# Kernel optimization log

Measured on AMD Instinct MI355X. Metric: run time of the kernel, lower is better.

## Reference

```python
import jax, jax.numpy as jnp
import numpy as np

N = 40000      # nodes
E = 640000     # edges (avg degree 16)
F = 128        # in_feats
OUT = 128      # out_feats


def setup_inputs() -> dict:
    key = jax.random.key(0)
    ks = jax.random.split(key, 8)
    feat = jax.random.normal(ks[0], (N, F), dtype=jnp.float32)
    src = jax.random.randint(ks[1], (E,), 0, N, dtype=jnp.int32)
    dst = jnp.sort(jax.random.randint(ks[2], (E,), 0, N, dtype=jnp.int32))
    # AttentionAGG: fc1 (2F -> F), fc2 (F -> 1); fc_layer (2F -> OUT)
    s1 = 1.0 / np.sqrt(2 * F)
    s2 = 1.0 / np.sqrt(F)
    w1 = jax.random.normal(ks[3], (2 * F, F), dtype=jnp.float32) * s1
    b1 = jnp.zeros((F,), dtype=jnp.float32)
    w2 = jax.random.normal(ks[4], (F, 1), dtype=jnp.float32) * s2
    b2 = jnp.zeros((1,), dtype=jnp.float32)
    wf = jax.random.normal(ks[5], (2 * F, OUT), dtype=jnp.float32) * s1
    bf = jnp.zeros((OUT,), dtype=jnp.float32)
    return {"feat": feat, "src": src, "dst": dst,
            "w1": w1, "b1": b1, "w2": w2, "b2": b2, "wf": wf, "bf": bf}


def reference(feat, src, dst, w1, b1, w2, b2, wf, bf):
    f = feat.shape[1]
    n = feat.shape[0]
    # fc1(concat(h_dst, m_src)) == h_dst @ w1[:F] + h_src @ w1[F:]  (edge_weight is None)
    proj_dst = feat @ w1[:f]          # [N, F]
    proj_src = feat @ w1[f:]          # [N, F]
    pre = jnp.tanh(proj_dst[dst] + proj_src[src] + b1)   # [E, F]
    scores = (pre @ w2)[:, 0] + b2[0]                    # [E]
    # softmax over the ragged incoming-edge set of each dst node
    smax = jax.ops.segment_max(scores, dst, num_segments=n, indices_are_sorted=True)
    ex = jnp.exp(scores - jax.lax.stop_gradient(smax)[dst])
    den = jax.ops.segment_sum(ex, dst, num_segments=n, indices_are_sorted=True)
    att = ex / den[dst]                                  # [E]
    # weighted segment-sum of messages (m_e = feat[src]); zero-degree nodes get 0
    neigh = jax.ops.segment_sum(att[:, None] * feat[src], dst,
                                num_segments=n, indices_are_sorted=True)  # [N, F]
    # fc_layer(concat(h_self, neigh))
    rst = feat @ wf[:f] + neigh @ wf[f:] + bf            # [N, OUT]
    return rst
```

## Files before the change

### kernel.cpp

```cpp
#include <hip/hip_runtime.h>
#include <math.h>

#define F 128
#define OUT 128

typedef unsigned short ushort_t;
typedef __attribute__((ext_vector_type(8))) short bfrag;
typedef __attribute__((ext_vector_type(4))) float ffrag;

__device__ __forceinline__ float bf_lo(unsigned int u) {
    return __uint_as_float(u << 16);
}
__device__ __forceinline__ float bf_hi(unsigned int u) {
    return __uint_as_float(u & 0xffff0000u);
}
__device__ __forceinline__ ushort_t f2bf(float f) {
    unsigned int x = __float_as_uint(f);
    unsigned int r = x + 0x7fffu + ((x >> 16) & 1u);
    return (ushort_t)(r >> 16);
}
__device__ __forceinline__ unsigned pk2(float lo, float hi) {
    return (unsigned)f2bf(lo) | ((unsigned)f2bf(hi) << 16);
}

#define DPP_ADD(x, ctrl) \
    ((x) + __int_as_float(__builtin_amdgcn_update_dpp( \
        0, __float_as_int(x), (ctrl), 0xf, 0xf, true)))

__global__ __launch_bounds__(256) void prep_kernel(
    const float* __restrict__ feat, const float* __restrict__ w1,
    const float* __restrict__ wf, const int* __restrict__ dst,
    ushort_t* __restrict__ abig, ushort_t* __restrict__ srcpack,
    ushort_t* __restrict__ btp, ushort_t* __restrict__ btf,
    int* __restrict__ row_ptr, int n, int e, int nb0, int nb1, int nb2)
{
    const int b = blockIdx.x, t = threadIdx.x;
    if (b < nb0) {
        int i = b * 256 + t;
        if (i >= n * 16) return;
        int row = i >> 4, c = (i & 15) * 8;
        float4 a = *(const float4*)(feat + (size_t)row * F + c);
        float4 bb = *(const float4*)(feat + (size_t)row * F + c + 4);
        unsigned p0 = pk2(a.x, a.y), p1 = pk2(a.z, a.w);
        unsigned p2 = pk2(bb.x, bb.y), p3 = pk2(bb.z, bb.w);
        *(uint4*)(abig + (size_t)row * 256 + c) = make_uint4(p0, p1, p2, p3);
        *(uint2*)(srcpack + (size_t)row * 256 + c * 2 + 4) = make_uint2(p0, p1);
        *(uint2*)(srcpack + (size_t)row * 256 + c * 2 + 12) = make_uint2(p2, p3);
    } else if (b < nb0 + nb1) {
        int idx = (b - nb0) * 256 + t;
        int j = idx >> 7, k = idx & 127;
        float v = (j < F) ? w1[(size_t)k * F + j]
                          : w1[(size_t)(F + k) * F + (j - F)];
        btp[idx] = f2bf(v);
    } else if (b < nb0 + nb1 + nb2) {
        int idx = (b - nb0 - nb1) * 256 + t;
        int j = idx >> 8, k = idx & 255;
        btf[idx] = f2bf(wf[(size_t)k * F + j]);
    } else {
        int i = (b - nb0 - nb1 - nb2) * 256 + t;
        if (i >= e) return;
        int d = dst[i];
        int prev = (i == 0) ? -1 : dst[i - 1];
        for (int v = prev + 1; v <= d; ++v) row_ptr[v] = i;
        if (i == e - 1) {
            for (int v = d + 1; v <= n; ++v) row_ptr[v] = e;
        }
    }
}

#define PST 136
__global__ __launch_bounds__(256) void proj_gemm_kernel(
    const ushort_t* __restrict__ abig, const ushort_t* __restrict__ btp,
    const float* __restrict__ b1, ushort_t* __restrict__ e_dst,
    ushort_t* __restrict__ srcpack, int n)
{
    __shared__ ushort_t As[64 * PST];
    __shared__ ushort_t Ep[4][16 * 80];
    const int t = threadIdx.x;
    const int wv = t >> 6, lane = t & 63;
    const int lm = lane & 15, quad = lane >> 4;
    const int row0 = blockIdx.x * 64, col0 = wv * 64;

#pragma unroll
    for (int k = 0; k < 4; ++k) {
        int l = k * 256 + t;
        int r = l >> 4, ch = l & 15;
        uint4 d = make_uint4(0, 0, 0, 0);
        if (row0 + r < n) d = *(const uint4*)(abig + (size_t)(row0 + r) * 256 + ch * 8);
        *(uint4*)(As + r * PST + ch * 8) = d;
    }
    __syncthreads();

    bfrag bfr[4][4];
#pragma unroll
    for (int ks = 0; ks < 4; ++ks)
#pragma unroll
        for (int ni = 0; ni < 4; ++ni)
            bfr[ks][ni] = *(const bfrag*)(btp + (size_t)(col0 + ni * 16 + lm) * 128
                                          + ks * 32 + quad * 8);

    ffrag acc[4][4];
#pragma unroll
    for (int mi = 0; mi < 4; ++mi)
#pragma unroll
        for (int ni = 0; ni < 4; ++ni) acc[mi][ni] = (ffrag){0.f, 0.f, 0.f, 0.f};

#pragma unroll
    for (int ks = 0; ks < 4; ++ks)
#pragma unroll
        for (int mi = 0; mi < 4; ++mi) {
            bfrag af = *(const bfrag*)(As + (mi * 16 + lm) * PST + ks * 32 + quad * 8);
#pragma unroll
            for (int ni = 0; ni < 4; ++ni)
                acc[mi][ni] = __builtin_amdgcn_mfma_f32_16x16x32_bf16(
                    af, bfr[ks][ni], acc[mi][ni], 0, 0, 0);
        }

    float bias[4];
#pragma unroll
    for (int ni = 0; ni < 4; ++ni)
        bias[ni] = (col0 < F) ? b1[col0 + ni * 16 + lm] : 0.f;

#pragma unroll
    for (int mi = 0; mi < 4; ++mi) {
#pragma unroll
        for (int ni = 0; ni < 4; ++ni)
#pragma unroll
            for (int r = 0; r < 4; ++r)
                Ep[wv][(quad * 4 + r) * 80 + ni * 16 + lm] =
                    f2bf(__expf(2.f * (acc[mi][ni][r] + bias[ni])));
#pragma unroll
        for (int ps = 0; ps < 2; ++ps) {
            int rl = ps * 8 + (lane >> 3), co = (lane & 7) * 8;
            uint4 vv = *(const uint4*)(&Ep[wv][rl * 80 + co]);
            int grow = row0 + mi * 16 + rl;
            if (grow < n) {
                if (col0 < F) {
                    *(uint4*)(e_dst + (size_t)grow * F + col0 + co) = vv;
                } else {
                    int f0 = col0 - F + co;
                    *(uint2*)(srcpack + (size_t)grow * 256 + f0 * 2) =
                        make_uint2(vv.x, vv.y);
                    *(uint2*)(srcpack + (size_t)grow * 256 + f0 * 2 + 8) =
                        make_uint2(vv.z, vv.w);
                }
            }
        }
    }
}

__global__ __launch_bounds__(256) void fused_kernel(
    const ushort_t* __restrict__ e_dst, const ushort_t* __restrict__ srcpack,
    const int* __restrict__ src, const int* __restrict__ row_ptr,
    const float* __restrict__ w2, ushort_t* __restrict__ abig, int n)
{
    const int v = (int)((blockIdx.x * 256u + threadIdx.x) >> 5);
    const int fl = threadIdx.x & 31;
    const int sbase = threadIdx.x & 32;

    const float4 wv4 = ((const float4*)w2)[fl];
    const float w0 = wv4.x, w1_ = wv4.y, w2_ = wv4.z, w3_ = wv4.w;
    float sw = w0 + w1_ + w2_ + w3_;
    float aw = fabsf(w0) + fabsf(w1_) + fabsf(w2_) + fabsf(w3_);
#pragma unroll
    for (int off = 16; off; off >>= 1) {
        sw += __shfl_xor(sw, off, 64);
        aw += __shfl_xor(aw, off, 64);
    }
    const float K = sw - aw;
    const float L2E = 1.4426950408889634f;
    const float K2 = K * L2E;

    if (v >= n) return;
    const int begin = row_ptr[v], end = row_ptr[v + 1];

    const uint2 ud = *(const uint2*)(e_dst + (size_t)v * F + fl * 4);
    const float ea0 = bf_lo(ud.x), ea1 = bf_hi(ud.x);
    const float ea2 = bf_lo(ud.y), ea3 = bf_hi(ud.y);

    const uint4* __restrict__ sp = (const uint4*)srcpack + fl;

    float s = 0.f, a0 = 0.f, a1 = 0.f, a2 = 0.f, a3 = 0.f;

    for (int cb = begin; cb < end; cb += 32) {
        const int clen = min(32, end - cb);
        const int sv = (fl < clen) ? src[cb + fl] : 0;
        int jj = 0;
        uint4 u[4];
        if (jj + 4 <= clen) {
#pragma unroll
            for (int q = 0; q < 4; ++q) {
                const int sq = __shfl(sv, sbase + q, 64);
                u[q] = sp[(size_t)sq * 32];
            }
        }
        while (jj + 4 <= clen) {
            const int jn = jj + 4;
            uint4 un[4];
            if (jn + 4 <= clen) {
#pragma unroll
                for (int q = 0; q < 4; ++q) {
                    const int sq = __shfl(sv, sbase + jn + q, 64);
                    un[q] = sp[(size_t)sq * 32];
                }
            }
            float p[4];
#pragma unroll
            for (int q = 0; q < 4; ++q) {
                float r;
                r = __builtin_amdgcn_rcpf(fmaf(ea0, bf_lo(u[q].x), 1.f)); p[q] = w0 * r;
                r = __builtin_amdgcn_rcpf(fmaf(ea1, bf_hi(u[q].x), 1.f)); p[q] = fmaf(w1_, r, p[q]);
                r = __builtin_amdgcn_rcpf(fmaf(ea2, bf_lo(u[q].y), 1.f)); p[q] = fmaf(w2_, r, p[q]);
                r = __builtin_amdgcn_rcpf(fmaf(ea3, bf_hi(u[q].y), 1.f)); p[q] = fmaf(w3_, r, p[q]);
            }
#pragma unroll
            for (int q = 0; q < 4; ++q) {
                p[q] = DPP_ADD(p[q], 0x121);
                p[q] = DPP_ADD(p[q], 0x122);
                p[q] = DPP_ADD(p[q], 0x124);
                p[q] = DPP_ADD(p[q], 0x128);
                p[q] += __shfl_xor(p[q], 16, 64);
            }
            float g[4];
#pragma unroll
            for (int q = 0; q < 4; ++q)
                g[q] = exp2f(fmaf(-2.f * L2E, p[q], K2));
            s += (g[0] + g[1]) + (g[2] + g[3]);
#pragma unroll
            for (int q = 0; q < 4; ++q) {
                a0 = fmaf(g[q], bf_lo(u[q].z), a0);
                a1 = fmaf(g[q], bf_hi(u[q].z), a1);
                a2 = fmaf(g[q], bf_lo(u[q].w), a2);
                a3 = fmaf(g[q], bf_hi(u[q].w), a3);
            }
            jj = jn;
            if (jj + 4 <= clen) {
#pragma unroll
                for (int q = 0; q < 4; ++q) u[q] = un[q];
            }
        }
        for (; jj < clen; ++jj) {
            const int s0 = __shfl(sv, sbase + jj, 64);
            const uint4 u0 = sp[(size_t)s0 * 32];
            float r, p0;
            r = __builtin_amdgcn_rcpf(fmaf(ea0, bf_lo(u0.x), 1.f)); p0 = w0 * r;
            r = __builtin_amdgcn_rcpf(fmaf(ea1, bf_hi(u0.x), 1.f)); p0 = fmaf(w1_, r, p0);
            r = __builtin_amdgcn_rcpf(fmaf(ea2, bf_lo(u0.y), 1.f)); p0 = fmaf(w2_, r, p0);
            r = __builtin_amdgcn_rcpf(fmaf(ea3, bf_hi(u0.y), 1.f)); p0 = fmaf(w3_, r, p0);
            p0 = DPP_ADD(p0, 0x121);
            p0 = DPP_ADD(p0, 0x122);
            p0 = DPP_ADD(p0, 0x124);
            p0 = DPP_ADD(p0, 0x128);
            p0 += __shfl_xor(p0, 16, 64);
            const float g0 = exp2f(fmaf(-2.f * L2E, p0, K2));
            s += g0;
            a0 = fmaf(g0, bf_lo(u0.z), a0);
            a1 = fmaf(g0, bf_hi(u0.z), a1);
            a2 = fmaf(g0, bf_lo(u0.w), a2);
            a3 = fmaf(g0, bf_hi(u0.w), a3);
        }
    }

    const float inv = (end > begin) ? 1.f / s : 0.f;
    ushort4 o = make_ushort4(f2bf(a0 * inv), f2bf(a1 * inv),
                             f2bf(a2 * inv), f2bf(a3 * inv));
    *(ushort4*)(abig + (size_t)v * 256 + 128 + fl * 4) = o;
}

#define OST 280
__global__ __launch_bounds__(256) void out_gemm_kernel(
    const ushort_t* __restrict__ abig, const ushort_t* __restrict__ btf,
    const float* __restrict__ bfv, float* __restrict__ out, int n)
{
    __shared__ ushort_t As[64 * OST];
    const int t = threadIdx.x;
    const int wv = t >> 6, lane = t & 63;
    const int lm = lane & 15, quad = lane >> 4;
    const int row0 = blockIdx.x * 64, col0 = wv * 32;

#pragma unroll
    for (int k = 0; k < 8; ++k) {
        int l = k * 256 + t;
        int r = l >> 5, ch = l & 31;
        uint4 d = make_uint4(0, 0, 0, 0);
        if (row0 + r < n) d = *(const uint4*)(abig + (size_t)(row0 + r) * 256 + ch * 8);
        *(uint4*)(As + r * OST + ch * 8) = d;
    }
    __syncthreads();

    bfrag bfr[8][2];
#pragma unroll
    for (int ks = 0; ks < 8; ++ks)
#pragma unroll
        for (int ni = 0; ni < 2; ++ni)
            bfr[ks][ni] = *(const bfrag*)(btf + (size_t)(col0 + ni * 16 + lm) * 256
                                          + ks * 32 + quad * 8);

    ffrag acc[4][2];
#pragma unroll
    for (int mi = 0; mi < 4; ++mi)
#pragma unroll
        for (int ni = 0; ni < 2; ++ni) acc[mi][ni] = (ffrag){0.f, 0.f, 0.f, 0.f};

#pragma unroll
    for (int ks = 0; ks < 8; ++ks)
#pragma unroll
        for (int mi = 0; mi < 4; ++mi) {
            bfrag af = *(const bfrag*)(As + (mi * 16 + lm) * OST + ks * 32 + quad * 8);
#pragma unroll
            for (int ni = 0; ni < 2; ++ni)
                acc[mi][ni] = __builtin_amdgcn_mfma_f32_16x16x32_bf16(
                    af, bfr[ks][ni], acc[mi][ni], 0, 0, 0);
        }

#pragma unroll
    for (int ni = 0; ni < 2; ++ni) {
        const int j = col0 + ni * 16 + lm;
        const float bb = bfv[j];
#pragma unroll
        for (int mi = 0; mi < 4; ++mi)
#pragma unroll
            for (int r = 0; r < 4; ++r) {
                int grow = row0 + mi * 16 + quad * 4 + r;
                if (grow < n) out[(size_t)grow * OUT + j] = acc[mi][ni][r] + bb;
            }
    }
}

extern "C" void kernel_launch(void* const* d_in, const int* in_sizes, int n_in,
                              void* d_out, int out_size, void* d_ws, size_t ws_size,
                              hipStream_t stream)
{
    const float* feat = (const float*)d_in[0];
    const int*   src  = (const int*)d_in[1];
    const int*   dst  = (const int*)d_in[2];
    const float* w1   = (const float*)d_in[3];
    const float* b1   = (const float*)d_in[4];
    const float* w2   = (const float*)d_in[5];
    const float* b2   = (const float*)d_in[6];  (void)b2;
    const float* wf   = (const float*)d_in[7];
    const float* bfv  = (const float*)d_in[8];
    float* out = (float*)d_out;

    const int n = in_sizes[0] / F;
    const int e = in_sizes[1];

    ushort_t* abig    = (ushort_t*)d_ws;
    ushort_t* e_dst   = abig + (size_t)n * 256;
    ushort_t* srcpack = e_dst + (size_t)n * 128;
    ushort_t* btp     = srcpack + (size_t)n * 256;
    ushort_t* btf     = btp + 32768;
    int* row_ptr      = (int*)(btf + 32768);

    const int nb0 = (n * 16 + 255) / 256;
    const int nb1 = 128, nb2 = 128;
    const int nb3 = (e + 255) / 256;

    prep_kernel<<<nb0 + nb1 + nb2 + nb3, 256, 0, stream>>>(
        feat, w1, wf, dst, abig, srcpack, btp, btf, row_ptr, n, e, nb0, nb1, nb2);
    proj_gemm_kernel<<<(n + 63) / 64, 256, 0, stream>>>(
        abig, btp, b1, e_dst, srcpack, n);
    fused_kernel<<<(n + 7) / 8, 256, 0, stream>>>(
        e_dst, srcpack, src, row_ptr, w2, abig, n);
    out_gemm_kernel<<<(n + 63) / 64, 256, 0, stream>>>(abig, btf, bfv, out, n);
}
```

Before: 169.9 us.

## Split fused attention kernel into separate score and aggregation kernels

Replaces the single fused edge kernel, which gathered an interleaved 16-byte src record holding projected and raw features, with two kernels. The score kernel gathers only the 8-byte projected src values and writes per-edge exp weights and the per-node reciprocal denominator to global memory. The aggregation kernel then gathers raw bf16 features from abig and accumulates the weighted sum. This removes the interleaved srcpack writes in prep and proj, but adds a kernel launch, a per-edge global round trip of the weights, and two separate random-gather passes. It also drops the software prefetch of the next edge group.

```diff
diff --git a/kernel.cpp b/kernel.cpp
--- a/kernel.cpp
+++ b/kernel.cpp
@@ -30,7 +30,7 @@
 __global__ __launch_bounds__(256) void prep_kernel(
     const float* __restrict__ feat, const float* __restrict__ w1,
     const float* __restrict__ wf, const int* __restrict__ dst,
-    ushort_t* __restrict__ abig, ushort_t* __restrict__ srcpack,
+    ushort_t* __restrict__ abig,
     ushort_t* __restrict__ btp, ushort_t* __restrict__ btf,
     int* __restrict__ row_ptr, int n, int e, int nb0, int nb1, int nb2)
 {
@@ -44,8 +44,6 @@
         unsigned p0 = pk2(a.x, a.y), p1 = pk2(a.z, a.w);
         unsigned p2 = pk2(bb.x, bb.y), p3 = pk2(bb.z, bb.w);
         *(uint4*)(abig + (size_t)row * 256 + c) = make_uint4(p0, p1, p2, p3);
-        *(uint2*)(srcpack + (size_t)row * 256 + c * 2 + 4) = make_uint2(p0, p1);
-        *(uint2*)(srcpack + (size_t)row * 256 + c * 2 + 12) = make_uint2(p2, p3);
     } else if (b < nb0 + nb1) {
         int idx = (b - nb0) * 256 + t;
         int j = idx >> 7, k = idx & 127;
@@ -72,7 +70,7 @@
 __global__ __launch_bounds__(256) void proj_gemm_kernel(
     const ushort_t* __restrict__ abig, const ushort_t* __restrict__ btp,
     const float* __restrict__ b1, ushort_t* __restrict__ e_dst,
-    ushort_t* __restrict__ srcpack, int n)
+    ushort_t* __restrict__ espack, int n)
 {
     __shared__ ushort_t As[64 * PST];
     __shared__ ushort_t Ep[4][16 * 80];
@@ -139,20 +137,18 @@
                     *(uint4*)(e_dst + (size_t)grow * F + col0 + co) = vv;
                 } else {
                     int f0 = col0 - F + co;
-                    *(uint2*)(srcpack + (size_t)grow * 256 + f0 * 2) =
-                        make_uint2(vv.x, vv.y);
-                    *(uint2*)(srcpack + (size_t)grow * 256 + f0 * 2 + 8) =
-                        make_uint2(vv.z, vv.w);
+                    *(uint4*)(espack + (size_t)grow * F + f0) = vv;
                 }
             }
         }
     }
 }
 
-__global__ __launch_bounds__(256) void fused_kernel(
-    const ushort_t* __restrict__ e_dst, const ushort_t* __restrict__ srcpack,
+__global__ __launch_bounds__(256) void score_kernel(
+    const ushort_t* __restrict__ e_dst, const ushort_t* __restrict__ espack,
     const int* __restrict__ src, const int* __restrict__ row_ptr,
-    const float* __restrict__ w2, ushort_t* __restrict__ abig, int n)
+    const float* __restrict__ w2, float* __restrict__ g_arr,
+    float* __restrict__ sden, int n)
 {
     const int v = (int)((blockIdx.x * 256u + threadIdx.x) >> 5);
     const int fl = threadIdx.x & 31;
@@ -178,31 +174,20 @@
     const float ea0 = bf_lo(ud.x), ea1 = bf_hi(ud.x);
     const float ea2 = bf_lo(ud.y), ea3 = bf_hi(ud.y);
 
-    const uint4* __restrict__ sp = (const uint4*)srcpack + fl;
-
-    float s = 0.f, a0 = 0.f, a1 = 0.f, a2 = 0.f, a3 = 0.f;
+    const uint2* __restrict__ sp = (const uint2*)espack + fl;
+
+    float s = 0.f;
 
     for (int cb = begin; cb < end; cb += 32) {
         const int clen = min(32, end - cb);
         const int sv = (fl < clen) ? src[cb + fl] : 0;
         int jj = 0;
-        uint4 u[4];
-        if (jj + 4 <= clen) {
-#pragma unroll
-            for (int q = 0; q < 4; ++q) {
-                const int sq = __shfl(sv, sbase + q, 64);
+        for (; jj + 4 <= clen; jj += 4) {
+            uint2 u[4];
+#pragma unroll
+            for (int q = 0; q < 4; ++q) {
+                const int sq = __shfl(sv, sbase + jj + q, 64);
                 u[q] = sp[(size_t)sq * 32];
-            }
-        }
-        while (jj + 4 <= clen) {
-            const int jn = jj + 4;
-            uint4 un[4];
-            if (jn + 4 <= clen) {
-#pragma unroll
-                for (int q = 0; q < 4; ++q) {
-                    const int sq = __shfl(sv, sbase + jn + q, 64);
-                    un[q] = sp[(size_t)sq * 32];
-                }
             }
             float p[4];
 #pragma unroll
@@ -221,27 +206,21 @@
                 p[q] = DPP_ADD(p[q], 0x128);
                 p[q] += __shfl_xor(p[q], 16, 64);
             }
-            float g[4];
-#pragma unroll
-            for (int q = 0; q < 4; ++q)
-                g[q] = exp2f(fmaf(-2.f * L2E, p[q], K2));
-            s += (g[0] + g[1]) + (g[2] + g[3]);
-#pragma unroll
-            for (int q = 0; q < 4; ++q) {
-                a0 = fmaf(g[q], bf_lo(u[q].z), a0);
-                a1 = fmaf(g[q], bf_hi(u[q].z), a1);
-                a2 = fmaf(g[q], bf_lo(u[q].w), a2);
-                a3 = fmaf(g[q], bf_hi(u[q].w), a3);
-            }
-            jj = jn;
-            if (jj + 4 <= clen) {
-#pragma unroll
-                for (int q = 0; q < 4; ++q) u[q] = un[q];
+            float g0 = exp2f(fmaf(-2.f * L2E, p[0], K2));
+            float g1 = exp2f(fmaf(-2.f * L2E, p[1], K2));
+            float g2 = exp2f(fmaf(-2.f * L2E, p[2], K2));
+            float g3 = exp2f(fmaf(-2.f * L2E, p[3], K2));
+            s += (g0 + g1) + (g2 + g3);
+            if (fl == 0) {
+                g_arr[cb + jj + 0] = g0;
+                g_arr[cb + jj + 1] = g1;
+                g_arr[cb + jj + 2] = g2;
+                g_arr[cb + jj + 3] = g3;
             }
         }
         for (; jj < clen; ++jj) {
             const int s0 = __shfl(sv, sbase + jj, 64);
-            const uint4 u0 = sp[(size_t)s0 * 32];
+            const uint2 u0 = sp[(size_t)s0 * 32];
             float r, p0;
             r = __builtin_amdgcn_rcpf(fmaf(ea0, bf_lo(u0.x), 1.f)); p0 = w0 * r;
             r = __builtin_amdgcn_rcpf(fmaf(ea1, bf_hi(u0.x), 1.f)); p0 = fmaf(w1_, r, p0);
@@ -252,16 +231,66 @@
             p0 = DPP_ADD(p0, 0x124);
             p0 = DPP_ADD(p0, 0x128);
             p0 += __shfl_xor(p0, 16, 64);
-            const float g0 = exp2f(fmaf(-2.f * L2E, p0, K2));
-            s += g0;
-            a0 = fmaf(g0, bf_lo(u0.z), a0);
-            a1 = fmaf(g0, bf_hi(u0.z), a1);
-            a2 = fmaf(g0, bf_lo(u0.w), a2);
-            a3 = fmaf(g0, bf_hi(u0.w), a3);
+            const float gg = exp2f(fmaf(-2.f * L2E, p0, K2));
+            s += gg;
+            if (fl == 0) g_arr[cb + jj] = gg;
         }
     }
 
     const float inv = (end > begin) ? 1.f / s : 0.f;
+    if (fl == 0) sden[v] = inv;
+}
+
+__global__ __launch_bounds__(256) void agg_kernel(
+    const int* __restrict__ src, const int* __restrict__ row_ptr,
+    const float* __restrict__ g_arr, const float* __restrict__ sden,
+    ushort_t* __restrict__ abig, int n)
+{
+    const int v = (int)((blockIdx.x * 256u + threadIdx.x) >> 5);
+    const int fl = threadIdx.x & 31;
+    const int sbase = threadIdx.x & 32;
+
+    if (v >= n) return;
+    const int begin = row_ptr[v], end = row_ptr[v + 1];
+    const float inv = sden[v];
+
+    const uint2* __restrict__ fp = (const uint2*)abig + fl;
+
+    float a0 = 0.f, a1 = 0.f, a2 = 0.f, a3 = 0.f;
+
+    for (int cb = begin; cb < end; cb += 32) {
+        const int clen = min(32, end - cb);
+        const int sv = (fl < clen) ? src[cb + fl] : 0;
+        int jj = 0;
+        for (; jj + 4 <= clen; jj += 4) {
+            uint2 u[4];
+            float g[4];
+#pragma unroll
+            for (int q = 0; q < 4; ++q) {
+                const int sq = __shfl(sv, sbase + jj + q, 64);
+                u[q] = fp[(size_t)sq * 64];
+            }
+#pragma unroll
+            for (int q = 0; q < 4; ++q) g[q] = g_arr[cb + jj + q];
+#pragma unroll
+            for (int q = 0; q < 4; ++q) {
+                a0 = fmaf(g[q], bf_lo(u[q].x), a0);
+                a1 = fmaf(g[q], bf_hi(u[q].x), a1);
+                a2 = fmaf(g[q], bf_lo(u[q].y), a2);
+                a3 = fmaf(g[q], bf_hi(u[q].y), a3);
+            }
+        }
+        for (; jj < clen; ++jj) {
+            const int s0 = __shfl(sv, sbase + jj, 64);
+            const uint2 u0 = fp[(size_t)s0 * 64];
+            const float gg = g_arr[cb + jj];
+            a0 = fmaf(gg, bf_lo(u0.x), a0);
+            a1 = fmaf(gg, bf_hi(u0.x), a1);
+            a2 = fmaf(gg, bf_lo(u0.y), a2);
+            a3 = fmaf(gg, bf_hi(u0.y), a3);
+        }
+    }
+
     ushort4 o = make_ushort4(f2bf(a0 * inv), f2bf(a1 * inv),
                              f2bf(a2 * inv), f2bf(a3 * inv));
     *(ushort4*)(abig + (size_t)v * 256 + 128 + fl * 4) = o;
@@ -347,20 +376,24 @@
 
     ushort_t* abig    = (ushort_t*)d_ws;
     ushort_t* e_dst   = abig + (size_t)n * 256;
-    ushort_t* srcpack = e_dst + (size_t)n * 128;
-    ushort_t* btp     = srcpack + (size_t)n * 256;
+    ushort_t* espack  = e_dst + (size_t)n * 128;
+    ushort_t* btp     = espack + (size_t)n * 128;
     ushort_t* btf     = btp + 32768;
     int* row_ptr      = (int*)(btf + 32768);
+    float* g_arr      = (float*)(row_ptr + n + 1);
+    float* sden       = g_arr + e;
 
     const int nb0 = (n * 16 + 255) / 256;
     const int nb1 = 128, nb2 = 128;
     const int nb3 = (e + 255) / 256;
 
     prep_kernel<<<nb0 + nb1 + nb2 + nb3, 256, 0, stream>>>(
-        feat, w1, wf, dst, abig, srcpack, btp, btf, row_ptr, n, e, nb0, nb1, nb2);
+        feat, w1, wf, dst, abig, btp, btf, row_ptr, n, e, nb0, nb1, nb2);
     proj_gemm_kernel<<<(n + 63) / 64, 256, 0, stream>>>(
-        abig, btp, b1, e_dst, srcpack, n);
-    fused_kernel<<<(n + 7) / 8, 256, 0, stream>>>(
-        e_dst, srcpack, src, row_ptr, w2, abig, n);
+        abig, btp, b1, e_dst, espack, n);
+    score_kernel<<<(n + 7) / 8, 256, 0, stream>>>(
+        e_dst, espack, src, row_ptr, w2, g_arr, sden, n);
+    agg_kernel<<<(n + 7) / 8, 256, 0, stream>>>(
+        src, row_ptr, g_arr, sden, abig, n);
     out_gemm_kernel<<<(n + 63) / 64, 256, 0, stream>>>(abig, btf, bfv, out, n);
 }
```

Measured after the change: 172.0 us. Within noise of the previous version (+1.3%).

## Grid-stride fused attention kernel, pair reciprocals, drop shuffle-based index prefetch

Applied to the files above, without the earlier changes.

The fused attention kernel now launches a fixed 1250 blocks and each 32-lane half-wave loops over nodes with a grid stride, instead of one half-wave per node. The score computation merges pairs of reciprocals into one rcp of a product (n/(AB) form), halving transcendental ops per edge. Source indices are now loaded directly per edge rather than coalesced into a register and shuffled, and the explicit software prefetch of the next four gathered rows is removed. This reduces per-edge ALU work and launch overhead but relies on the compiler or occupancy to hide gather latency, and the product form risks overflow or precision loss.

```diff
diff --git a/kernel.cpp b/kernel.cpp
--- a/kernel.cpp
+++ b/kernel.cpp
@@ -152,11 +152,10 @@
 __global__ __launch_bounds__(256) void fused_kernel(
     const ushort_t* __restrict__ e_dst, const ushort_t* __restrict__ srcpack,
     const int* __restrict__ src, const int* __restrict__ row_ptr,
-    const float* __restrict__ w2, ushort_t* __restrict__ abig, int n)
-{
-    const int v = (int)((blockIdx.x * 256u + threadIdx.x) >> 5);
+    const float* __restrict__ w2, ushort_t* __restrict__ abig, int n, int nhw)
+{
+    const int hw0 = (int)((blockIdx.x * 256u + threadIdx.x) >> 5);
     const int fl = threadIdx.x & 31;
-    const int sbase = threadIdx.x & 32;
 
     const float4 wv4 = ((const float4*)w2)[fl];
     const float w0 = wv4.x, w1_ = wv4.y, w2_ = wv4.z, w3_ = wv4.w;
@@ -171,47 +170,37 @@
     const float L2E = 1.4426950408889634f;
     const float K2 = K * L2E;
 
-    if (v >= n) return;
-    const int begin = row_ptr[v], end = row_ptr[v + 1];
-
-    const uint2 ud = *(const uint2*)(e_dst + (size_t)v * F + fl * 4);
-    const float ea0 = bf_lo(ud.x), ea1 = bf_hi(ud.x);
-    const float ea2 = bf_lo(ud.y), ea3 = bf_hi(ud.y);
-
     const uint4* __restrict__ sp = (const uint4*)srcpack + fl;
 
-    float s = 0.f, a0 = 0.f, a1 = 0.f, a2 = 0.f, a3 = 0.f;
-
-    for (int cb = begin; cb < end; cb += 32) {
-        const int clen = min(32, end - cb);
-        const int sv = (fl < clen) ? src[cb + fl] : 0;
-        int jj = 0;
-        uint4 u[4];
-        if (jj + 4 <= clen) {
+    for (int v = hw0; v < n; v += nhw) {
+        const int begin = row_ptr[v], end = row_ptr[v + 1];
+
+        const uint2 ud = *(const uint2*)(e_dst + (size_t)v * F + fl * 4);
+        const float ea0 = bf_lo(ud.x), ea1 = bf_hi(ud.x);
+        const float ea2 = bf_lo(ud.y), ea3 = bf_hi(ud.y);
+
+        float s = 0.f, a0 = 0.f, a1 = 0.f, a2 = 0.f, a3 = 0.f;
+
+        int ee = begin;
+        for (; ee + 4 <= end; ee += 4) {
+            uint4 u[4];
 #pragma unroll
             for (int q = 0; q < 4; ++q) {
-                const int sq = __shfl(sv, sbase + q, 64);
+                const int sq = src[ee + q];
                 u[q] = sp[(size_t)sq * 32];
             }
-        }
-        while (jj + 4 <= clen) {
-            const int jn = jj + 4;
-            uint4 un[4];
-            if (jn + 4 <= clen) {
-#pragma unroll
-                for (int q = 0; q < 4; ++q) {
-                    const int sq = __shfl(sv, sbase + jn + q, 64);
-                    un[q] = sp[(size_t)sq * 32];
-                }
-            }
             float p[4];
 #pragma unroll
             for (int q = 0; q < 4; ++q) {
-                float r;
-                r = __builtin_amdgcn_rcpf(fmaf(ea0, bf_lo(u[q].x), 1.f)); p[q] = w0 * r;
-                r = __builtin_amdgcn_rcpf(fmaf(ea1, bf_hi(u[q].x), 1.f)); p[q] = fmaf(w1_, r, p[q]);
-                r = __builtin_amdgcn_rcpf(fmaf(ea2, bf_lo(u[q].y), 1.f)); p[q] = fmaf(w2_, r, p[q]);
-                r = __builtin_amdgcn_rcpf(fmaf(ea3, bf_hi(u[q].y), 1.f)); p[q] = fmaf(w3_, r, p[q]);
+                float A = fmaf(ea0, bf_lo(u[q].x), 1.f);
+                float B = fmaf(ea1, bf_hi(u[q].x), 1.f);
+                float C = fmaf(ea2, bf_lo(u[q].y), 1.f);
+                float D = fmaf(ea3, bf_hi(u[q].y), 1.f);
+                float nAB = fmaf(w0, B, w1_ * A);
+                float nCD = fmaf(w2_, D, w3_ * C);
+                float rAB = __builtin_amdgcn_rcpf(A * B);
+                float rCD = __builtin_amdgcn_rcpf(C * D);
+                p[q] = fmaf(nAB, rAB, nCD * rCD);
             }
 #pragma unroll
             for (int q = 0; q < 4; ++q) {
@@ -233,20 +222,19 @@
                 a2 = fmaf(g[q], bf_lo(u[q].w), a2);
                 a3 = fmaf(g[q], bf_hi(u[q].w), a3);
             }
-            jj = jn;
-            if (jj + 4 <= clen) {
-#pragma unroll
-                for (int q = 0; q < 4; ++q) u[q] = un[q];
-            }
-        }
-        for (; jj < clen; ++jj) {
-            const int s0 = __shfl(sv, sbase + jj, 64);
+        }
+        for (; ee < end; ++ee) {
+            const int s0 = src[ee];
             const uint4 u0 = sp[(size_t)s0 * 32];
-            float r, p0;
-            r = __builtin_amdgcn_rcpf(fmaf(ea0, bf_lo(u0.x), 1.f)); p0 = w0 * r;
-            r = __builtin_amdgcn_rcpf(fmaf(ea1, bf_hi(u0.x), 1.f)); p0 = fmaf(w1_, r, p0);
-            r = __builtin_amdgcn_rcpf(fmaf(ea2, bf_lo(u0.y), 1.f)); p0 = fmaf(w2_, r, p0);
-            r = __builtin_amdgcn_rcpf(fmaf(ea3, bf_hi(u0.y), 1.f)); p0 = fmaf(w3_, r, p0);
+            float A = fmaf(ea0, bf_lo(u0.x), 1.f);
+            float B = fmaf(ea1, bf_hi(u0.x), 1.f);
+            float C = fmaf(ea2, bf_lo(u0.y), 1.f);
+            float D = fmaf(ea3, bf_hi(u0.y), 1.f);
+            float nAB = fmaf(w0, B, w1_ * A);
+            float nCD = fmaf(w2_, D, w3_ * C);
+            float rAB = __builtin_amdgcn_rcpf(A * B);
+            float rCD = __builtin_amdgcn_rcpf(C * D);
+            float p0 = fmaf(nAB, rAB, nCD * rCD);
             p0 = DPP_ADD(p0, 0x121);
             p0 = DPP_ADD(p0, 0x122);
             p0 = DPP_ADD(p0, 0x124);
@@ -259,12 +247,12 @@
             a2 = fmaf(g0, bf_lo(u0.w), a2);
             a3 = fmaf(g0, bf_hi(u0.w), a3);
         }
-    }
-
-    const float inv = (end > begin) ? 1.f / s : 0.f;
-    ushort4 o = make_ushort4(f2bf(a0 * inv), f2bf(a1 * inv),
-                             f2bf(a2 * inv), f2bf(a3 * inv));
-    *(ushort4*)(abig + (size_t)v * 256 + 128 + fl * 4) = o;
+
+        const float inv = (end > begin) ? 1.f / s : 0.f;
+        ushort4 o = make_ushort4(f2bf(a0 * inv), f2bf(a1 * inv),
+                                 f2bf(a2 * inv), f2bf(a3 * inv));
+        *(ushort4*)(abig + (size_t)v * 256 + 128 + fl * 4) = o;
+    }
 }
 
 #define OST 280
@@ -356,11 +344,14 @@
     const int nb1 = 128, nb2 = 128;
     const int nb3 = (e + 255) / 256;
 
+    const int fblocks = 1250;
+    const int nhw = fblocks * 8;
+
     prep_kernel<<<nb0 + nb1 + nb2 + nb3, 256, 0, stream>>>(
         feat, w1, wf, dst, abig, srcpack, btp, btf, row_ptr, n, e, nb0, nb1, nb2);
     proj_gemm_kernel<<<(n + 63) / 64, 256, 0, stream>>>(
         abig, btp, b1, e_dst, srcpack, n);
-    fused_kernel<<<(n + 7) / 8, 256, 0, stream>>>(
-        e_dst, srcpack, src, row_ptr, w2, abig, n);
+    fused_kernel<<<fblocks, 256, 0, stream>>>(
+        e_dst, srcpack, src, row_ptr, w2, abig, n, nhw);
     out_gemm_kernel<<<(n + 63) / 64, 256, 0, stream>>>(abig, btf, bfv, out, n);
 }
```

New measurement: 170.8 us. Within noise of the previous version (+0.5%).
